# Kernel optimization log

Hardware: AMD Instinct MI355X
Metric: run time of the kernel (lower is better)

The kernel has to match this reference:

```python
import jax, jax.numpy as jnp
import numpy as np

DIM = 768
N_HEADS = 12
HEAD_DIM = DIM // N_HEADS
MAX_REL = 3  # hardcoded in the module


def setup_inputs() -> dict:
    key = jax.random.key(0)
    ks = jax.random.split(key, 10)
    B, L = 4, 1024
    def xavier(k, shape):
        fan_in, fan_out = shape[-2], shape[-1]
        a = jnp.sqrt(6.0 / (fan_in + fan_out))
        return jax.random.uniform(k, shape, jnp.float32, -a, a)
    return {
        "query": jax.random.normal(ks[0], (B, L, DIM), jnp.float32),
        "key":   jax.random.normal(ks[1], (B, L, DIM), jnp.float32),
        "value": jax.random.normal(ks[2], (B, L, DIM), jnp.float32),
        "Wq": xavier(ks[3], (DIM, DIM)),
        "Wk": xavier(ks[4], (DIM, DIM)),
        "Wv": xavier(ks[5], (DIM, DIM)),
        "Wproj": xavier(ks[6], (DIM, DIM)),
        "b_proj": jnp.zeros((DIM,), jnp.float32),
        "rel_k_table": xavier(ks[7], (2 * MAX_REL + 1, HEAD_DIM)),
        "rel_v_table": xavier(ks[8], (2 * MAX_REL + 1, HEAD_DIM)),
    }


def _rel_embed(table, len_q, len_k):
    # [len_q, len_k, head_dim] gathered from clipped relative distances
    dist = jnp.arange(len_k)[None, :] - jnp.arange(len_q)[:, None]
    idx = jnp.clip(dist, -MAX_REL, MAX_REL) + MAX_REL
    return table[idx]


def reference(query, key, value, Wq, Wk, Wv, Wproj, b_proj, rel_k_table, rel_v_table):
    B, Lq, _ = query.shape
    Lk = key.shape[1]
    H, hd = N_HEADS, HEAD_DIM
    scale = hd ** (-0.5)

    q = query @ Wq.T                      # [B, Lq, D]
    k = key @ Wk.T                        # [B, Lk, D]
    v = value @ Wv.T                      # [B, Lk, D]

    qh = q.reshape(B, Lq, H, hd).transpose(0, 2, 1, 3)   # [B,H,Lq,hd]
    kh = k.reshape(B, Lk, H, hd).transpose(0, 2, 1, 3)
    vh = v.reshape(B, Lk, H, hd).transpose(0, 2, 1, 3)

    # content-content scores
    attn1 = jnp.einsum('bhqd,bhkd->bhqk', qh, kh)
    # content-relative-position scores
    rk = _rel_embed(rel_k_table, Lq, Lk)                  # [Lq,Lk,hd]
    attn2 = jnp.einsum('bhqd,qkd->bhqk', qh, rk)
    # NOTE: original code DIVIDES by scale (= hd**-0.5), i.e. multiplies by sqrt(hd)
    attn = (attn1 + attn2) / scale
    attn = jax.nn.softmax(attn, axis=-1)                  # [B,H,Lq,Lk]

    w1 = jnp.einsum('bhqk,bhkd->bhqd', attn, vh)
    rv = _rel_embed(rel_v_table, Lq, Lk)                  # [Lq,Lk,hd]
    w2 = jnp.einsum('bhqk,qkd->bhqd', attn, rv)

    x = (w1 + w2).transpose(0, 2, 1, 3).reshape(B, Lq, H * hd)
    x = x @ Wproj.T + b_proj
    return (x, attn)
```

## Files before the change

### kernel.cpp

```cpp
#include <hip/hip_runtime.h>

#define DIMM 768
#define NH 12
#define HD 64
#define LSEQ 1024
#define BATCH 4
#define NXE 3145728
#define NWE 589824

typedef __bf16 bf16x8 __attribute__((ext_vector_type(8)));
typedef float f32x4 __attribute__((ext_vector_type(4)));
typedef unsigned short u16;

static __device__ __forceinline__ u16 f2bf(float f) {
  unsigned u = __builtin_bit_cast(unsigned, f);
  u += 0x7fffu + ((u >> 16) & 1u);
  return (u16)(u >> 16);
}
static __device__ __forceinline__ float bf2f(u16 h) {
  unsigned u = ((unsigned)h) << 16;
  return __builtin_bit_cast(float, u);
}
static __device__ __forceinline__ bf16x8 ld8bf(const u16* p) {
  uint4 u = *(const uint4*)p;
  return __builtin_bit_cast(bf16x8, u);
}
#define MFMA(a, b, c) __builtin_amdgcn_mfma_f32_16x16x32_bf16(a, b, c, 0, 0, 0)
#define GLL(g, s)                                                      \
  __builtin_amdgcn_global_load_lds(                                    \
      (const __attribute__((address_space(1))) void*)(g),              \
      (__attribute__((address_space(3))) void*)(s), 16, 0, 0)

__global__ __launch_bounds__(256) void convert(
    const float* __restrict__ q_in, const float* __restrict__ k_in,
    const float* __restrict__ v_in, const float* __restrict__ Wq,
    const float* __restrict__ Wk, const float* __restrict__ Wv,
    const float* __restrict__ Wp, u16* __restrict__ AqH, u16* __restrict__ AqL,
    u16* __restrict__ AkH, u16* __restrict__ AkL, u16* __restrict__ Av,
    u16* __restrict__ WqH, u16* __restrict__ WqL, u16* __restrict__ WkH,
    u16* __restrict__ WkL, u16* __restrict__ Wvr, u16* __restrict__ Wpr) {
  long i = ((long)blockIdx.x * 256 + threadIdx.x) * 4;
  const float* src;
  u16 *dh, *dl = nullptr;
  long off;
  if (i < NXE) { src = q_in; dh = AqH; dl = AqL; off = i; }
  else if (i < 2L * NXE) { src = k_in; dh = AkH; dl = AkL; off = i - NXE; }
  else if (i < 3L * NXE) { src = v_in; dh = Av; off = i - 2L * NXE; }
  else {
    long j = i - 3L * NXE;
    int which = (int)(j / NWE);
    off = j % NWE;
    if (which == 0) { src = Wq; dh = WqH; dl = WqL; }
    else if (which == 1) { src = Wk; dh = WkH; dl = WkL; }
    else if (which == 2) { src = Wv; dh = Wvr; }
    else { src = Wp; dh = Wpr; }
  }
  float4 v = *(const float4*)(src + off);
  ushort4 h;
  h.x = f2bf(v.x); h.y = f2bf(v.y); h.z = f2bf(v.z); h.w = f2bf(v.w);
  *(ushort4*)(dh + off) = h;
  if (dl) {
    ushort4 lo;
    lo.x = f2bf(v.x - bf2f(h.x)); lo.y = f2bf(v.y - bf2f(h.y));
    lo.z = f2bf(v.z - bf2f(h.z)); lo.w = f2bf(v.w - bf2f(h.w));
    *(ushort4*)(dl + off) = lo;
  }
}

__global__ __launch_bounds__(256, 4) void gemm_multi(
    int mode0, const u16* __restrict__ AqH, const u16* __restrict__ AqL,
    const u16* __restrict__ AkH, const u16* __restrict__ AkL,
    const u16* __restrict__ Av, const u16* __restrict__ WqH,
    const u16* __restrict__ WqL, const u16* __restrict__ WkH,
    const u16* __restrict__ WkL, const u16* __restrict__ Wvr,
    const u16* __restrict__ Wpr, const u16* __restrict__ wbuf,
    u16* __restrict__ qhi, u16* __restrict__ qlo, u16* __restrict__ khi,
    u16* __restrict__ klo, u16* __restrict__ vT, float* __restrict__ outp,
    const float* __restrict__ bias) {
  __shared__ u16 sAh[64 * 32], sAl[64 * 32];
  __shared__ u16 sBh[128 * 32], sBl[128 * 32];
  const int mode = mode0 + blockIdx.z;
  const u16 *Ah, *Al = nullptr, *Bh, *Bl = nullptr;
  if (mode == 0) { Ah = AqH; Al = AqL; Bh = WqH; Bl = WqL; }
  else if (mode == 1) { Ah = AkH; Al = AkL; Bh = WkH; Bl = WkL; }
  else if (mode == 2) { Ah = Av; Bh = Wvr; }
  else { Ah = wbuf; Bh = Wpr; }
  const int t = threadIdx.x, w = t >> 6, l = t & 63;
  const int quad = l >> 4, l15 = l & 15;
  const int m0 = blockIdx.x * 64, n0 = blockIdx.y * 128;
  const int wm = (w & 1) * 32, wn = (w >> 1) * 64;
  const int srow = t >> 2, scol = (t & 3) * 8;
  const u16* gA = Ah + (m0 + srow) * DIMM + scol;
  const u16* gB = Bh + (n0 + srow) * DIMM + scol;
  const u16* gAl = (mode < 2) ? Al + (m0 + srow) * DIMM + scol : nullptr;
  const u16* gBl = (mode < 2) ? Bl + (n0 + srow) * DIMM + scol : nullptr;
  u16* lA = sAh + w * 512;
  u16* lB = sBh + w * 512;
  u16* lAl = sAl + w * 512;
  u16* lBl = sBl + w * 512;
  f32x4 acc[2][4] = {};

#define STAGE_G(k0)                                                    \
  do {                                                                 \
    GLL(gA + (k0), lA);                                                \
    GLL(gB + (k0), lB);                                                \
    GLL(gB + 64 * DIMM + (k0), lB + 2048);                             \
    if (mode < 2) {                                                    \
      GLL(gAl + (k0), lAl);                                            \
      GLL(gBl + (k0), lBl);                                            \
      GLL(gBl + 64 * DIMM + (k0), lBl + 2048);                         \
    }                                                                  \
  } while (0)

  STAGE_G(0);
  if (mode < 2) {
    for (int k0 = 0; k0 < DIMM; k0 += 32) {
      __syncthreads();
      bf16x8 ah[2], al[2], bh[4], bl[4];
#pragma unroll
      for (int i = 0; i < 2; ++i) {
        ah[i] = __builtin_bit_cast(
            bf16x8, *(const uint4*)(sAh + (wm + i * 16 + l15) * 32 + quad * 8));
        al[i] = __builtin_bit_cast(
            bf16x8, *(const uint4*)(sAl + (wm + i * 16 + l15) * 32 + quad * 8));
      }
#pragma unroll
      for (int j = 0; j < 4; ++j) {
        bh[j] = __builtin_bit_cast(
            bf16x8, *(const uint4*)(sBh + (wn + j * 16 + l15) * 32 + quad * 8));
        bl[j] = __builtin_bit_cast(
            bf16x8, *(const uint4*)(sBl + (wn + j * 16 + l15) * 32 + quad * 8));
      }
      __syncthreads();
      if (k0 + 32 < DIMM) STAGE_G(k0 + 32);
#pragma unroll
      for (int i = 0; i < 2; ++i)
#pragma unroll
        for (int j = 0; j < 4; ++j) acc[i][j] = MFMA(ah[i], bh[j], acc[i][j]);
#pragma unroll
      for (int i = 0; i < 2; ++i)
#pragma unroll
        for (int j = 0; j < 4; ++j) acc[i][j] = MFMA(al[i], bh[j], acc[i][j]);
#pragma unroll
      for (int i = 0; i < 2; ++i)
#pragma unroll
        for (int j = 0; j < 4; ++j) acc[i][j] = MFMA(ah[i], bl[j], acc[i][j]);
    }
  } else {
    for (int k0 = 0; k0 < DIMM; k0 += 32) {
      __syncthreads();
      bf16x8 ah[2], bh[4];
#pragma unroll
      for (int i = 0; i < 2; ++i)
        ah[i] = __builtin_bit_cast(
            bf16x8, *(const uint4*)(sAh + (wm + i * 16 + l15) * 32 + quad * 8));
#pragma unroll
      for (int j = 0; j < 4; ++j)
        bh[j] = __builtin_bit_cast(
            bf16x8, *(const uint4*)(sBh + (wn + j * 16 + l15) * 32 + quad * 8));
      __syncthreads();
      if (k0 + 32 < DIMM) STAGE_G(k0 + 32);
#pragma unroll
      for (int i = 0; i < 2; ++i)
#pragma unroll
        for (int j = 0; j < 4; ++j) acc[i][j] = MFMA(ah[i], bh[j], acc[i][j]);
    }
  }
#undef STAGE_G

  u16* oh = (mode == 0) ? qhi : khi;
  u16* ol = (mode == 0) ? qlo : klo;
#pragma unroll
  for (int i = 0; i < 2; ++i)
#pragma unroll
    for (int j = 0; j < 4; ++j)
#pragma unroll
      for (int r = 0; r < 4; ++r) {
        int grow = m0 + wm + i * 16 + quad * 4 + r;
        int gcol = n0 + wn + j * 16 + l15;
        float c = acc[i][j][r];
        int b = grow >> 10, ll = grow & 1023, h = gcol >> 6, d = gcol & 63;
        if (mode < 2) {
          int idx = ((b * NH + h) * LSEQ + ll) * HD + d;
          u16 hi = f2bf(c);
          oh[idx] = hi;
          ol[idx] = f2bf(c - bf2f(hi));
        } else if (mode == 2) {
          vT[((b * NH + h) * HD + d) * LSEQ + ll] = f2bf(c);
        } else {
          outp[grow * DIMM + gcol] = c + bias[gcol];
        }
      }
}

__global__ __launch_bounds__(256, 3) void attn_core(
    const u16* __restrict__ qhi, const u16* __restrict__ qlo,
    const u16* __restrict__ khi, const u16* __restrict__ klo,
    const u16* __restrict__ vT, const float* __restrict__ relk,
    const float* __restrict__ relv, float* __restrict__ attn_out,
    u16* __restrict__ wbuf) {
  __shared__ __align__(16) u16 uni[16 * 1032];
  __shared__ float qrel[16][7];
  __shared__ float arel[16][7];
  __shared__ float rvt[7][64];
  __shared__ float red[4][16][4];

  const int Lb = blockIdx.x + 64 * (blockIdx.y + NH * blockIdx.z);
  const int flat = (Lb & 7) * 384 + (Lb >> 3);
  const int qt = flat & 63, h = (flat >> 6) % NH, b = flat / (64 * NH);
  const int q0 = qt * 16;
  const int tid = threadIdx.x, wave = tid >> 6, lane = tid & 63;
  const int quad = lane >> 4, l15 = lane & 15;
  const int bhd = b * NH + h;

  const int rs = tid >> 3;
  const int cg = (tid & 7) ^ (rs & 7);
  const u16* gh = khi + (bhd * LSEQ + rs) * HD + cg * 8;
  const u16* gl = klo + (bhd * LSEQ + rs) * HD + cg * 8;
  u16* const wslot = uni + tid * 8;
  const int rowA = wave * 16 + l15;
  const int sw = rowA & 7;
  const int s0 = (rowA * 8 + (quad ^ sw)) * 8;
  const int s1 = (rowA * 8 + ((quad + 4) ^ sw)) * 8;

  uint4 sA0, sA1, sA2, sA3, sB0, sB1, sB2, sB3;
#define LOADA(c)                                                     \
  do {                                                               \
    sA0 = *(const uint4*)(gh + (c) * (64 * HD));                     \
    sA1 = *(const uint4*)(gh + (c) * (64 * HD) + 32 * HD);           \
    sA2 = *(const uint4*)(gl + (c) * (64 * HD));                     \
    sA3 = *(const uint4*)(gl + (c) * (64 * HD) + 32 * HD);           \
  } while (0)
#define LOADB(c)                                                     \
  do {                                                               \
    sB0 = *(const uint4*)(gh + (c) * (64 * HD));                     \
    sB1 = *(const uint4*)(gh + (c) * (64 * HD) + 32 * HD);           \
    sB2 = *(const uint4*)(gl + (c) * (64 * HD));                     \
    sB3 = *(const uint4*)(gl + (c) * (64 * HD) + 32 * HD);           \
  } while (0)
#define DSWRITE_A(bufsel)                                            \
  do {                                                               \
    u16* d_ = wslot + (bufsel) * 8192;                               \
    *(uint4*)(d_) = sA0;                                             \
    *(uint4*)(d_ + 2048) = sA1;                                      \
    *(uint4*)(d_ + 4096) = sA2;                                      \
    *(uint4*)(d_ + 6144) = sA3;                                      \
  } while (0)
#define DSWRITE_B(bufsel)                                            \
  do {                                                               \
    u16* d_ = wslot + (bufsel) * 8192;                               \
    *(uint4*)(d_) = sB0;                                             \
    *(uint4*)(d_ + 2048) = sB1;                                      \
    *(uint4*)(d_ + 4096) = sB2;                                      \
    *(uint4*)(d_ + 6144) = sB3;                                      \
  } while (0)

  const int qbase = (bhd * LSEQ + q0 + l15) * HD + quad * 8;
  bf16x8 ah0 = ld8bf(qhi + qbase);
  bf16x8 ah1 = ld8bf(qhi + qbase + 32);
  bf16x8 al0 = ld8bf(qlo + qbase);
  bf16x8 al1 = ld8bf(qlo + qbase + 32);
  LOADA(0);
  LOADB(1);

  for (int t = tid; t < 7 * HD; t += 256) rvt[t >> 6][t & 63] = relv[t];
  if (tid < 112) {
    int q = tid / 7, rr = tid % 7;
    const u16* qp = qhi + (bhd * LSEQ + q0 + q) * HD;
    const u16* lp = qlo + (bhd * LSEQ + q0 + q) * HD;
    const float* tp = relk + rr * HD;
    float s = 0.f;
#pragma unroll
    for (int d8 = 0; d8 < HD; d8 += 8) {
      uint4 uh = *(const uint4*)(qp + d8);
      uint4 ul = *(const uint4*)(lp + d8);
      float4 t0 = *(const float4*)(tp + d8);
      float4 t1 = *(const float4*)(tp + d8 + 4);
      unsigned hh[4] = {uh.x, uh.y, uh.z, uh.w};
      unsigned lv[4] = {ul.x, ul.y, ul.z, ul.w};
      float tv[8] = {t0.x, t0.y, t0.z, t0.w, t1.x, t1.y, t1.z, t1.w};
#pragma unroll
      for (int m = 0; m < 4; ++m) {
        s += (bf2f((u16)(hh[m] & 0xffff)) + bf2f((u16)(lv[m] & 0xffff))) * tv[2 * m];
        s += (bf2f((u16)(hh[m] >> 16)) + bf2f((u16)(lv[m] >> 16))) * tv[2 * m + 1];
      }
    }
    qrel[q][rr] = s;
    arel[q][rr] = 0.f;
  }

  DSWRITE_A(0);
  asm volatile("s_waitcnt lgkmcnt(0)" ::: "memory");
  __builtin_amdgcn_sched_barrier(0);
  __builtin_amdgcn_s_barrier();

  f32x4 sc[16];
#pragma unroll
  for (int c = 0; c < 16; ++c) {
    const u16* cur = uni + (c & 1) * 8192;
    bf16x8 kh0 = ld8bf(cur + s0);
    bf16x8 kh1 = ld8bf(cur + s1);
    bf16x8 kl0 = ld8bf(cur + 4096 + s0);
    bf16x8 kl1 = ld8bf(cur + 4096 + s1);
    f32x4 e = {}, f = {};
    e = MFMA(ah0, kh0, e);
    f = MFMA(ah1, kh1, f);
    e = MFMA(ah0, kl0, e);
    f = MFMA(ah1, kl1, f);
    e = MFMA(al0, kh0, e);
    f = MFMA(al1, kh1, f);
    sc[c] = e + f;
    if (c < 14) {
      if ((c & 1) == 0) LOADA(c + 2); else LOADB(c + 2);
    }
    if (c < 15) {
      if ((c & 1) == 0) DSWRITE_B(1); else DSWRITE_A(0);
      asm volatile("s_waitcnt lgkmcnt(0)" ::: "memory");
      __builtin_amdgcn_sched_barrier(0);
      __builtin_amdgcn_s_barrier();
    }
  }
#undef LOADA
#undef LOADB
#undef DSWRITE_A
#undef DSWRITE_B

  const int colbase = wave * 16 + l15;
  const int dbase = colbase - q0 - quad * 4;
  float mrow[4] = {-3.4e38f, -3.4e38f, -3.4e38f, -3.4e38f};
#pragma unroll
  for (int c = 0; c < 16; ++c)
#pragma unroll
    for (int r = 0; r < 4; ++r) {
      int d = dbase + c * 64 - r;
      int ri = d < -3 ? 0 : (d > 3 ? 6 : d + 3);
      float s = (sc[c][r] + qrel[quad * 4 + r][ri]) * 8.0f;
      sc[c][r] = s;
      mrow[r] = fmaxf(mrow[r], s);
    }
#pragma unroll
  for (int m = 1; m <= 8; m <<= 1)
#pragma unroll
    for (int r = 0; r < 4; ++r) mrow[r] = fmaxf(mrow[r], __shfl_xor(mrow[r], m));
  if (l15 < 4) {
    float mv = l15 == 0 ? mrow[0] : l15 == 1 ? mrow[1] : l15 == 2 ? mrow[2] : mrow[3];
    red[0][quad * 4 + l15][wave] = mv;
  }
  __syncthreads();
  float mx[4];
#pragma unroll
  for (int r = 0; r < 4; ++r) {
    int row = quad * 4 + r;
    mx[r] = fmaxf(fmaxf(red[0][row][0], red[0][row][1]),
                  fmaxf(red[0][row][2], red[0][row][3]));
  }

  float sum[4] = {}, s0a[4] = {}, s6a[4] = {};
#pragma unroll
  for (int c = 0; c < 16; ++c)
#pragma unroll
    for (int r = 0; r < 4; ++r) {
      float e = __expf(sc[c][r] - mx[r]);
      sc[c][r] = e;
      int d = dbase + c * 64 - r;
      sum[r] += e;
      if (d <= -3) s0a[r] += e;
      if (d >= 3) s6a[r] += e;
    }
#pragma unroll
  for (int m = 1; m <= 8; m <<= 1)
#pragma unroll
    for (int r = 0; r < 4; ++r) {
      sum[r] += __shfl_xor(sum[r], m);
      s0a[r] += __shfl_xor(s0a[r], m);
      s6a[r] += __shfl_xor(s6a[r], m);
    }
  if (l15 < 4) {
    int row = quad * 4 + l15;
    float sv = l15 == 0 ? sum[0] : l15 == 1 ? sum[1] : l15 == 2 ? sum[2] : sum[3];
    float a0 = l15 == 0 ? s0a[0] : l15 == 1 ? s0a[1] : l15 == 2 ? s0a[2] : s0a[3];
    float a6 = l15 == 0 ? s6a[0] : l15 == 1 ? s6a[1] : l15 == 2 ? s6a[2] : s6a[3];
    red[1][row][wave] = sv;
    red[2][row][wave] = a0;
    red[3][row][wave] = a6;
  }
  __syncthreads();
  float rn[4];
#pragma unroll
  for (int r = 0; r < 4; ++r) {
    int row = quad * 4 + r;
    float s = red[1][row][0] + red[1][row][1] + red[1][row][2] + red[1][row][3];
    rn[r] = 1.0f / s;
    if (wave == 0 && l15 == 0) {
      float t0 = red[2][row][0] + red[2][row][1] + red[2][row][2] + red[2][row][3];
      float t6 = red[3][row][0] + red[3][row][1] + red[3][row][2] + red[3][row][3];
      arel[row][0] = t0 * rn[r];
      arel[row][6] = t6 * rn[r];
    }
  }

#pragma unroll
  for (int c = 0; c < 16; ++c) {
    int col = colbase + c * 64;
#pragma unroll
    for (int r = 0; r < 4; ++r) {
      int row = quad * 4 + r;
      float p = sc[c][r] * rn[r];
      uni[row * 1032 + col] = f2bf(p);
      int d = dbase + c * 64 - r;
      if (d >= -2 && d <= 2) arel[row][d + 3] = p;
    }
  }
  __syncthreads();

  {
    float* aob = attn_out + ((size_t)(bhd * LSEQ + q0)) * LSEQ;
#pragma unroll
    for (int row = 0; row < 16; ++row) {
      uint2 u = *(const uint2*)&uni[row * 1032 + tid * 4];
      float4 f = {bf2f((u16)(u.x & 0xffff)), bf2f((u16)(u.x >> 16)),
                  bf2f((u16)(u.y & 0xffff)), bf2f((u16)(u.y >> 16))};
      *(float4*)(aob + row * LSEQ + tid * 4) = f;
    }
  }

  {
    const u16* vb = vT + (bhd * HD + wave * 16 + l15) * LSEQ;
    f32x4 acc0 = {}, acc1 = {};
#pragma unroll 4
    for (int kk = 0; kk < LSEQ; kk += 64) {
      int ak = kk + quad * 8;
      bf16x8 aP0 = __builtin_bit_cast(bf16x8, *(const uint4*)&uni[l15 * 1032 + ak]);
      bf16x8 bV0 = ld8bf(vb + ak);
      acc0 = MFMA(aP0, bV0, acc0);
      bf16x8 aP1 = __builtin_bit_cast(bf16x8, *(const uint4*)&uni[l15 * 1032 + ak + 32]);
      bf16x8 bV1 = ld8bf(vb + ak + 32);
      acc1 = MFMA(aP1, bV1, acc1);
    }
    f32x4 acc = acc0 + acc1;
    const int col = wave * 16 + l15;
#pragma unroll
    for (int r = 0; r < 4; ++r) {
      int row = quad * 4 + r;
      float w2 = 0.f;
#pragma unroll
      for (int t = 0; t < 7; ++t) w2 += arel[row][t] * rvt[t][col];
      wbuf[(b * LSEQ + q0 + row) * DIMM + h * HD + col] = f2bf(acc[r] + w2);
    }
  }
}

extern "C" void kernel_launch(void* const* d_in, const int* in_sizes, int n_in,
                              void* d_out, int out_size, void* d_ws, size_t ws_size,
                              hipStream_t stream) {
  const float* q_in = (const float*)d_in[0];
  const float* k_in = (const float*)d_in[1];
  const float* v_in = (const float*)d_in[2];
  const float* Wq = (const float*)d_in[3];
  const float* Wk = (const float*)d_in[4];
  const float* Wv = (const float*)d_in[5];
  const float* Wp = (const float*)d_in[6];
  const float* bias = (const float*)d_in[7];
  const float* relk = (const float*)d_in[8];
  const float* relv = (const float*)d_in[9];
  float* out = (float*)d_out;

  u16* p = (u16*)d_ws;
  u16 *AqH = p, *AqL = AqH + NXE, *AkH = AqL + NXE, *AkL = AkH + NXE,
      *Av = AkL + NXE;
  u16 *WqH = Av + NXE, *WqL = WqH + NWE, *WkH = WqL + NWE, *WkL = WkH + NWE,
      *Wvr = WkL + NWE, *Wpr = Wvr + NWE;
  u16 *qhi = Wpr + NWE, *qlo = qhi + NXE, *khi = qlo + NXE, *klo = khi + NXE,
      *vT = klo + NXE, *wbuf = vT + NXE;

  convert<<<(3 * NXE + 4 * NWE) / 1024, 256, 0, stream>>>(
      q_in, k_in, v_in, Wq, Wk, Wv, Wp, AqH, AqL, AkH, AkL, Av, WqH, WqL, WkH,
      WkL, Wvr, Wpr);
  gemm_multi<<<dim3(64, 6, 3), 256, 0, stream>>>(
      0, AqH, AqL, AkH, AkL, Av, WqH, WqL, WkH, WkL, Wvr, Wpr, wbuf, qhi, qlo,
      khi, klo, vT, out, bias);
  attn_core<<<dim3(64, NH, BATCH), 256, 0, stream>>>(
      qhi, qlo, khi, klo, vT, relk, relv, out + NXE, wbuf);
  gemm_multi<<<dim3(64, 6, 1), 256, 0, stream>>>(
      3, AqH, AqL, AkH, AkL, Av, WqH, WqL, WkH, WkL, Wvr, Wpr, wbuf, qhi, qlo,
      khi, klo, vT, out, bias);
}
```

Measured before the change: 430.0 us.

## Register-prefetch GEMM pipeline, swizzle block order, split QKV/proj kernels

Replaces the direct global-to-LDS loads in the projection GEMM with a register-staged software pipeline. Tiles for step k+2 are loaded into registers while step k's tile is consumed, and explicit waitcnt plus s_barrier fences replace __syncthreads. It also swizzles the block-to-tile mapping for L2 locality and splits the kernel into separate QKV and projection entry points so the projection mode is a compile-time constant. Costs are extra VGPRs for the staged tiles and hand-managed synchronization that must order the LDS reads and writes correctly.

After: 427.8 us. About the same (-0.5%).

```diff
diff --git a/kernel.cpp b/kernel.cpp
--- a/kernel.cpp
+++ b/kernel.cpp
@@ -26,10 +26,12 @@
   return __builtin_bit_cast(bf16x8, u);
 }
 #define MFMA(a, b, c) __builtin_amdgcn_mfma_f32_16x16x32_bf16(a, b, c, 0, 0, 0)
-#define GLL(g, s)                                                      \
-  __builtin_amdgcn_global_load_lds(                                    \
-      (const __attribute__((address_space(1))) void*)(g),              \
-      (__attribute__((address_space(3))) void*)(s), 16, 0, 0)
+#define LGKM0_FENCE()                                      \
+  do {                                                     \
+    asm volatile("s_waitcnt lgkmcnt(0)" ::: "memory");     \
+    __builtin_amdgcn_sched_barrier(0);                     \
+    __builtin_amdgcn_s_barrier();                          \
+  } while (0)
 
 __global__ __launch_bounds__(256) void convert(
     const float* __restrict__ q_in, const float* __restrict__ k_in,
@@ -67,19 +69,14 @@
   }
 }
 
-__global__ __launch_bounds__(256, 4) void gemm_multi(
-    int mode0, const u16* __restrict__ AqH, const u16* __restrict__ AqL,
-    const u16* __restrict__ AkH, const u16* __restrict__ AkL,
-    const u16* __restrict__ Av, const u16* __restrict__ WqH,
-    const u16* __restrict__ WqL, const u16* __restrict__ WkH,
-    const u16* __restrict__ WkL, const u16* __restrict__ Wvr,
-    const u16* __restrict__ Wpr, const u16* __restrict__ wbuf,
-    u16* __restrict__ qhi, u16* __restrict__ qlo, u16* __restrict__ khi,
-    u16* __restrict__ klo, u16* __restrict__ vT, float* __restrict__ outp,
-    const float* __restrict__ bias) {
+__device__ __forceinline__ void gemm_body(
+    int mode, const u16* AqH, const u16* AqL, const u16* AkH, const u16* AkL,
+    const u16* Av, const u16* WqH, const u16* WqL, const u16* WkH,
+    const u16* WkL, const u16* Wvr, const u16* Wpr, const u16* wbuf,
+    u16* qhi, u16* qlo, u16* khi, u16* klo, u16* vT, float* outp,
+    const float* bias) {
   __shared__ u16 sAh[64 * 32], sAl[64 * 32];
   __shared__ u16 sBh[128 * 32], sBl[128 * 32];
-  const int mode = mode0 + blockIdx.z;
   const u16 *Ah, *Al = nullptr, *Bh, *Bl = nullptr;
   if (mode == 0) { Ah = AqH; Al = AqL; Bh = WqH; Bl = WqL; }
   else if (mode == 1) { Ah = AkH; Al = AkL; Bh = WkH; Bl = WkL; }
@@ -87,35 +84,43 @@
   else { Ah = wbuf; Bh = Wpr; }
   const int t = threadIdx.x, w = t >> 6, l = t & 63;
   const int quad = l >> 4, l15 = l & 15;
-  const int m0 = blockIdx.x * 64, n0 = blockIdx.y * 128;
+  const int flat = blockIdx.x + 64 * blockIdx.y;
+  const int swz = (flat & 7) * 48 + (flat >> 3);
+  const int m0 = (swz & 63) * 64, n0 = (swz >> 6) * 128;
   const int wm = (w & 1) * 32, wn = (w >> 1) * 64;
   const int srow = t >> 2, scol = (t & 3) * 8;
+  const int t8 = t * 8;
   const u16* gA = Ah + (m0 + srow) * DIMM + scol;
   const u16* gB = Bh + (n0 + srow) * DIMM + scol;
   const u16* gAl = (mode < 2) ? Al + (m0 + srow) * DIMM + scol : nullptr;
   const u16* gBl = (mode < 2) ? Bl + (n0 + srow) * DIMM + scol : nullptr;
-  u16* lA = sAh + w * 512;
-  u16* lB = sBh + w * 512;
-  u16* lAl = sAl + w * 512;
-  u16* lBl = sBl + w * 512;
   f32x4 acc[2][4] = {};
-
-#define STAGE_G(k0)                                                    \
-  do {                                                                 \
-    GLL(gA + (k0), lA);                                                \
-    GLL(gB + (k0), lB);                                                \
-    GLL(gB + 64 * DIMM + (k0), lB + 2048);                             \
-    if (mode < 2) {                                                    \
-      GLL(gAl + (k0), lAl);                                            \
-      GLL(gBl + (k0), lBl);                                            \
-      GLL(gBl + 64 * DIMM + (k0), lBl + 2048);                         \
-    }                                                                  \
-  } while (0)
-
-  STAGE_G(0);
+  uint4 rA, rB0, rB1, rAl, rBl0, rBl1;
+
   if (mode < 2) {
+#define LOADS2(k0n)                                                  \
+    do {                                                             \
+      rA = *(const uint4*)(gA + (k0n));                              \
+      rB0 = *(const uint4*)(gB + (k0n));                             \
+      rB1 = *(const uint4*)(gB + 64 * DIMM + (k0n));                 \
+      rAl = *(const uint4*)(gAl + (k0n));                            \
+      rBl0 = *(const uint4*)(gBl + (k0n));                           \
+      rBl1 = *(const uint4*)(gBl + 64 * DIMM + (k0n));               \
+    } while (0)
+#define DSW2()                                                       \
+    do {                                                             \
+      *(uint4*)(sAh + t8) = rA;                                      \
+      *(uint4*)(sBh + t8) = rB0;                                     \
+      *(uint4*)(sBh + t8 + 2048) = rB1;                              \
+      *(uint4*)(sAl + t8) = rAl;                                     \
+      *(uint4*)(sBl + t8) = rBl0;                                    \
+      *(uint4*)(sBl + t8 + 2048) = rBl1;                             \
+    } while (0)
+    LOADS2(0);
+    DSW2();
+    LOADS2(32);
+    LGKM0_FENCE();
     for (int k0 = 0; k0 < DIMM; k0 += 32) {
-      __syncthreads();
       bf16x8 ah[2], al[2], bh[4], bl[4];
 #pragma unroll
       for (int i = 0; i < 2; ++i) {
@@ -131,8 +136,11 @@
         bl[j] = __builtin_bit_cast(
             bf16x8, *(const uint4*)(sBl + (wn + j * 16 + l15) * 32 + quad * 8));
       }
-      __syncthreads();
-      if (k0 + 32 < DIMM) STAGE_G(k0 + 32);
+      LGKM0_FENCE();
+      if (k0 < DIMM - 32) {
+        DSW2();
+        if (k0 < DIMM - 64) LOADS2(k0 + 64);
+      }
 #pragma unroll
       for (int i = 0; i < 2; ++i)
 #pragma unroll
@@ -145,10 +153,28 @@
       for (int i = 0; i < 2; ++i)
 #pragma unroll
         for (int j = 0; j < 4; ++j) acc[i][j] = MFMA(ah[i], bl[j], acc[i][j]);
-    }
+      if (k0 < DIMM - 32) LGKM0_FENCE();
+    }
+#undef LOADS2
+#undef DSW2
   } else {
+#define LOADS1(k0n)                                                  \
+    do {                                                             \
+      rA = *(const uint4*)(gA + (k0n));                              \
+      rB0 = *(const uint4*)(gB + (k0n));                             \
+      rB1 = *(const uint4*)(gB + 64 * DIMM + (k0n));                 \
+    } while (0)
+#define DSW1()                                                       \
+    do {                                                             \
+      *(uint4*)(sAh + t8) = rA;                                      \
+      *(uint4*)(sBh + t8) = rB0;                                     \
+      *(uint4*)(sBh + t8 + 2048) = rB1;                              \
+    } while (0)
+    LOADS1(0);
+    DSW1();
+    LOADS1(32);
+    LGKM0_FENCE();
     for (int k0 = 0; k0 < DIMM; k0 += 32) {
-      __syncthreads();
       bf16x8 ah[2], bh[4];
 #pragma unroll
       for (int i = 0; i < 2; ++i)
@@ -158,15 +184,20 @@
       for (int j = 0; j < 4; ++j)
         bh[j] = __builtin_bit_cast(
             bf16x8, *(const uint4*)(sBh + (wn + j * 16 + l15) * 32 + quad * 8));
-      __syncthreads();
-      if (k0 + 32 < DIMM) STAGE_G(k0 + 32);
+      LGKM0_FENCE();
+      if (k0 < DIMM - 32) {
+        DSW1();
+        if (k0 < DIMM - 64) LOADS1(k0 + 64);
+      }
 #pragma unroll
       for (int i = 0; i < 2; ++i)
 #pragma unroll
         for (int j = 0; j < 4; ++j) acc[i][j] = MFMA(ah[i], bh[j], acc[i][j]);
-    }
-  }
-#undef STAGE_G
+      if (k0 < DIMM - 32) LGKM0_FENCE();
+    }
+#undef LOADS1
+#undef DSW1
+  }
 
   u16* oh = (mode == 0) ? qhi : khi;
   u16* ol = (mode == 0) ? qlo : klo;
@@ -191,6 +222,34 @@
           outp[grow * DIMM + gcol] = c + bias[gcol];
         }
       }
+}
+
+__global__ __launch_bounds__(256, 4) void gemm_qkv(
+    const u16* __restrict__ AqH, const u16* __restrict__ AqL,
+    const u16* __restrict__ AkH, const u16* __restrict__ AkL,
+    const u16* __restrict__ Av, const u16* __restrict__ WqH,
+    const u16* __restrict__ WqL, const u16* __restrict__ WkH,
+    const u16* __restrict__ WkL, const u16* __restrict__ Wvr,
+    const u16* __restrict__ Wpr, const u16* __restrict__ wbuf,
+    u16* __restrict__ qhi, u16* __restrict__ qlo, u16* __restrict__ khi,
+    u16* __restrict__ klo, u16* __restrict__ vT, float* __restrict__ outp,
+    const float* __restrict__ bias) {
+  gemm_body(blockIdx.z, AqH, AqL, AkH, AkL, Av, WqH, WqL, WkH, WkL, Wvr, Wpr,
+            wbuf, qhi, qlo, khi, klo, vT, outp, bias);
+}
+
+__global__ __launch_bounds__(256, 4) void gemm_proj(
+    const u16* __restrict__ AqH, const u16* __restrict__ AqL,
+    const u16* __restrict__ AkH, const u16* __restrict__ AkL,
+    const u16* __restrict__ Av, const u16* __restrict__ WqH,
+    const u16* __restrict__ WqL, const u16* __restrict__ WkH,
+    const u16* __restrict__ WkL, const u16* __restrict__ Wvr,
+    const u16* __restrict__ Wpr, const u16* __restrict__ wbuf,
+    u16* __restrict__ qhi, u16* __restrict__ qlo, u16* __restrict__ khi,
+    u16* __restrict__ klo, u16* __restrict__ vT, float* __restrict__ outp,
+    const float* __restrict__ bias) {
+  gemm_body(3, AqH, AqL, AkH, AkL, Av, WqH, WqL, WkH, WkL, Wvr, Wpr,
+            wbuf, qhi, qlo, khi, klo, vT, outp, bias);
 }
 
 __global__ __launch_bounds__(256, 3) void attn_core(
@@ -476,12 +535,12 @@
   convert<<<(3 * NXE + 4 * NWE) / 1024, 256, 0, stream>>>(
       q_in, k_in, v_in, Wq, Wk, Wv, Wp, AqH, AqL, AkH, AkL, Av, WqH, WqL, WkH,
       WkL, Wvr, Wpr);
-  gemm_multi<<<dim3(64, 6, 3), 256, 0, stream>>>(
-      0, AqH, AqL, AkH, AkL, Av, WqH, WqL, WkH, WkL, Wvr, Wpr, wbuf, qhi, qlo,
+  gemm_qkv<<<dim3(64, 6, 3), 256, 0, stream>>>(
+      AqH, AqL, AkH, AkL, Av, WqH, WqL, WkH, WkL, Wvr, Wpr, wbuf, qhi, qlo,
       khi, klo, vT, out, bias);
   attn_core<<<dim3(64, NH, BATCH), 256, 0, stream>>>(
       qhi, qlo, khi, klo, vT, relk, relv, out + NXE, wbuf);
-  gemm_multi<<<dim3(64, 6, 1), 256, 0, stream>>>(
-      3, AqH, AqL, AkH, AkL, Av, WqH, WqL, WkH, WkL, Wvr, Wpr, wbuf, qhi, qlo,
+  gemm_proj<<<dim3(64, 6, 1), 256, 0, stream>>>(
+      AqH, AqL, AkH, AkL, Av, WqH, WqL, WkH, WkL, Wvr, Wpr, wbuf, qhi, qlo,
       khi, klo, vT, out, bias);
 }
```
